# Performance work log

Measured on AMD Instinct MI355X. Metric: run time of the kernel, lower is better.

Reference implementation:

```python
import jax, jax.numpy as jnp
import numpy as np

B, N = 8, 512
EMBED, EDGE_D, FLAG_D = 256, 32, 32
NODE_NUM, EDGE_NUM, FLAG_NUM = 20000, 16, 4
IN_DIM = 2 * EMBED + 2 * FLAG_D + EDGE_D  # concat order: [head_emb, tail_emb, head_flag, tail_flag, edge]
NEG = -1e12


def setup_inputs() -> dict:
    key = jax.random.key(0)
    ks = jax.random.split(key, 16)
    s = 0.05
    return {
        "adjacent_matrix": jax.random.randint(ks[0], (B, N, N), 0, 2, dtype=jnp.int32),
        "head_nodes": jax.random.randint(ks[1], (B, N), 0, NODE_NUM, dtype=jnp.int32),
        "head_flag_bit_matrix": jax.random.randint(ks[2], (B, N), 0, FLAG_NUM, dtype=jnp.int32),
        "edge_type_matrix": jax.random.randint(ks[3], (B, N, N), 0, EDGE_NUM, dtype=jnp.int32),
        "node_emb": jax.random.normal(ks[4], (NODE_NUM, EMBED)) * s,
        "edge_emb": jax.random.normal(ks[5], (EDGE_NUM, EDGE_D)) * s,
        "flag_emb": jax.random.normal(ks[6], (FLAG_NUM, FLAG_D)) * s,
        "t1_w": jax.random.normal(ks[7], (EMBED, EMBED)) * s,
        "t1_b": jax.random.normal(ks[8], (EMBED,)) * s,
        "w1": jax.random.normal(ks[9], (IN_DIM,)) * s,
        "b1": jax.random.normal(ks[10], ()) * s,
        "t2_w": jax.random.normal(ks[11], (EMBED, EMBED)) * s,
        "t2_b": jax.random.normal(ks[12], (EMBED,)) * s,
        "w2": jax.random.normal(ks[13], (IN_DIM,)) * s,
        "b2": jax.random.normal(ks[14], ()) * s,
    }


def _leaky_relu(x):
    return jnp.where(x > 0, x, 0.1 * x)


def _gat_layer(h, f, e, adj, w, b):
    # Decompose Linear(concat([h_i, h_j, f_i, f_j, e_ij])) into per-part dot
    # products summed by broadcasting -> avoids the [B,N,N,IN_DIM] concat.
    D, F = h.shape[-1], f.shape[-1]
    wh, wt = w[:D], w[D:2 * D]
    wfh, wft = w[2 * D:2 * D + F], w[2 * D + F:2 * D + 2 * F]
    we = w[2 * D + 2 * F:]
    logit = ((h @ wh)[:, :, None] + (h @ wt)[:, None, :]
             + (f @ wfh)[:, :, None] + (f @ wft)[:, None, :]
             + jnp.einsum('bije,e->bij', e, we) + b)  # [B,N,N]
    logit = _leaky_relu(logit)
    logit = jnp.where(adj == 0, NEG, logit)
    att = jax.nn.softmax(logit, axis=1)  # softmax over head axis i
    # out[b,j] = sum_i att[b,i,j] * h[b,i]   (== bmm(att^T, h))
    return jnp.einsum('bij,bid->bjd', att, h)


def reference(adjacent_matrix, head_nodes, head_flag_bit_matrix, edge_type_matrix,
              node_emb, edge_emb, flag_emb,
              t1_w, t1_b, w1, b1, t2_w, t2_b, w2, b2):
    h = node_emb[head_nodes] @ t1_w.T + t1_b          # [B,N,D] (t1 projection)
    f = flag_emb[head_flag_bit_matrix]                # [B,N,F]
    e = edge_emb[edge_type_matrix]                    # [B,N,N,E]
    t = _gat_layer(h, f, e, adjacent_matrix, w1, b1)  # layer 1 aggregate
    t = jax.nn.sigmoid(t)
    h2 = t @ t2_w.T + t2_b                            # t2 projection
    return _gat_layer(h2, f, e, adjacent_matrix, w2, b2)
```

## Files before the change

kernel.cpp:

```cpp
#include <hip/hip_runtime.h>
#include <hip/hip_bf16.h>

#define BB 8
#define NN 512
#define DD 256
#define NROWS (BB*NN)
#define JT 16

using bf16x8 = __attribute__((ext_vector_type(8))) short;
using f32x4  = __attribute__((ext_vector_type(4))) float;
typedef unsigned short us_t;

__device__ __forceinline__ us_t f2bf(float x) {
    union { float f; unsigned int u; } v; v.f = x;
    unsigned int r = (v.u + 0x7fffu + ((v.u >> 16) & 1u)) >> 16;
    return (us_t)r;
}

__global__ __launch_bounds__(256) void prep_w(
    const float* __restrict__ w1f, const float* __restrict__ w2f,
    us_t* __restrict__ o1, us_t* __restrict__ o2)
{
    int i = blockIdx.x*1024 + threadIdx.x*4;
    float4 a = *(const float4*)(w1f + i);
    float4 b = *(const float4*)(w2f + i);
    ushort4 u;
    u.x = f2bf(a.x); u.y = f2bf(a.y); u.z = f2bf(a.z); u.w = f2bf(a.w);
    *(ushort4*)&o1[i] = u;
    u.x = f2bf(b.x); u.y = f2bf(b.y); u.z = f2bf(b.z); u.w = f2bf(b.w);
    *(ushort4*)&o2[i] = u;
}

__device__ __forceinline__ void lin_body(
    int bid, int t,
    const us_t* __restrict__ Wbf, const float* __restrict__ bias,
    const float* __restrict__ Xf, const int* __restrict__ idx,
    const float* __restrict__ wvec, const int* __restrict__ flagidx,
    const float* __restrict__ flag_emb,
    us_t* __restrict__ hT, float* __restrict__ aout, float* __restrict__ cout,
    float* redA, float* redC)
{
    const int wave = t >> 6, lane = t & 63;
    const int lrow = lane & 15, kg = lane >> 4;
    const int r0 = bid * 16;
    const int dw = wave * 64;

    const int arow = r0 + lrow;
    const int nid = idx ? idx[arow] : arow;

    f32x4 acc[4];
    #pragma unroll
    for (int n = 0; n < 4; ++n) acc[n] = (f32x4){0.f, 0.f, 0.f, 0.f};

    const float4* xr = (const float4*)(Xf + (size_t)nid * DD);
    #pragma unroll
    for (int ks = 0; ks < DD/32; ++ks) {
        float4 xa = xr[ks*8 + kg*2];
        float4 xb = xr[ks*8 + kg*2 + 1];
        bf16x8 af;
        af[0] = (short)f2bf(xa.x); af[1] = (short)f2bf(xa.y);
        af[2] = (short)f2bf(xa.z); af[3] = (short)f2bf(xa.w);
        af[4] = (short)f2bf(xb.x); af[5] = (short)f2bf(xb.y);
        af[6] = (short)f2bf(xb.z); af[7] = (short)f2bf(xb.w);
        #pragma unroll
        for (int n = 0; n < 4; ++n) {
            bf16x8 bfr = *(const bf16x8*)(Wbf + (size_t)(dw + n*16 + lrow)*DD
                                           + ks*32 + kg*8);
            acc[n] = __builtin_amdgcn_mfma_f32_16x16x32_bf16(af, bfr, acc[n], 0, 0, 0);
        }
    }

    const int b  = r0 >> 9;
    const int i0 = (r0 & 511) + kg*4;
    float pa[4] = {0.f,0.f,0.f,0.f}, pc[4] = {0.f,0.f,0.f,0.f};
    #pragma unroll
    for (int n = 0; n < 4; ++n) {
        int d = dw + n*16 + lrow;
        float bv = bias[d];
        float whd = wvec[d], wtd = wvec[256+d];
        ushort4 u;
        #pragma unroll
        for (int r = 0; r < 4; ++r) {
            float v = acc[n][r] + bv;
            ((us_t*)&u)[r] = f2bf(v);
            pa[r] += v * whd;
            pc[r] += v * wtd;
        }
        *(ushort4*)&hT[(size_t)b*DD*NN + (size_t)d*NN + i0] = u;
    }
    #pragma unroll
    for (int r = 0; r < 4; ++r) {
        #pragma unroll
        for (int m = 1; m < 16; m <<= 1) {
            pa[r] += __shfl_xor(pa[r], m);
            pc[r] += __shfl_xor(pc[r], m);
        }
    }
    if (lrow == 0) {
        #pragma unroll
        for (int r = 0; r < 4; ++r) {
            redA[wave*16 + kg*4 + r] = pa[r];
            redC[wave*16 + kg*4 + r] = pc[r];
        }
    }
    __syncthreads();
    if (t < 128) {
        const int m = t >> 3, sub = t & 7;
        const int fi = flagidx[r0 + m];
        float fa = 0.f, fc = 0.f;
        #pragma unroll
        for (int q = 0; q < 4; ++q) {
            int e = sub*4 + q;
            float fe = flag_emb[fi*32 + e];
            fa += fe * wvec[512 + e];
            fc += fe * wvec[544 + e];
        }
        #pragma unroll
        for (int mm = 1; mm < 8; mm <<= 1) {
            fa += __shfl_xor(fa, mm);
            fc += __shfl_xor(fc, mm);
        }
        if (sub == 0) {
            float sa = fa, sc = fc;
            #pragma unroll
            for (int wv = 0; wv < 4; ++wv) { sa += redA[wv*16 + m]; sc += redC[wv*16 + m]; }
            aout[r0 + m] = sa;
            cout[r0 + m] = sc;
        }
    }
}

__global__ __launch_bounds__(256) void k1(
    const us_t* __restrict__ Wb1, const float* __restrict__ bias1,
    const float* __restrict__ node_emb, const int* __restrict__ head_nodes,
    const float* __restrict__ wvec1, const int* __restrict__ flagidx,
    const float* __restrict__ flag_emb,
    us_t* __restrict__ hT, float* __restrict__ a1, float* __restrict__ c1,
    const int* __restrict__ adj, const int* __restrict__ et,
    unsigned char* __restrict__ pk)
{
    __shared__ float redA[64], redC[64];
    const int blk = blockIdx.x, t = threadIdx.x;
    if (blk < 256) {
        lin_body(blk, t, Wb1, bias1, node_emb, head_nodes,
                 wvec1, flagidx, flag_emb, hT, a1, c1, redA, redC);
    } else {
        int g = ((blk - 256)*256 + t)*4;
        int4 av = *(const int4*)(adj + g);
        int4 ev = *(const int4*)(et + g);
        uchar4 u;
        u.x = (unsigned char)((ev.x&15)|(av.x<<4));
        u.y = (unsigned char)((ev.y&15)|(av.y<<4));
        u.z = (unsigned char)((ev.z&15)|(av.z<<4));
        u.w = (unsigned char)((ev.w&15)|(av.w<<4));
        *(uchar4*)(pk + g) = u;
    }
}

__global__ __launch_bounds__(256) void attn1_lin2(
    const unsigned char* __restrict__ pk,
    const float* __restrict__ edge_emb, const float* __restrict__ w,
    const float* __restrict__ bptr,
    const float* __restrict__ a, const float* __restrict__ c,
    const us_t* __restrict__ hT,
    const us_t* __restrict__ Wb2, const float* __restrict__ bias2,
    const float* __restrict__ wvec2, const int* __restrict__ flagidx,
    const float* __restrict__ flag_emb,
    us_t* __restrict__ hT2, float* __restrict__ a2, float* __restrict__ c2)
{
    __shared__ __align__(16) float p[NN][JT+1];
    __shared__ __align__(16) us_t Pb[JT][NN+8];
    __shared__ __align__(16) us_t Sg[16][DD+8];
    __shared__ float as[NN];
    __shared__ float edot[16];
    __shared__ float cjs[JT];
    __shared__ float red[16][JT];
    __shared__ float mj[JT];
    __shared__ float invden[JT];
    __shared__ float redA[64], redC[64];

    const int t = threadIdx.x;
    const int b  = blockIdx.x >> 5;
    const int j0 = (blockIdx.x & 31) * JT;

    as[t]       = a[b*NN + t];
    as[256 + t] = a[b*NN + 256 + t];
    if (t < 16) {
        float s = 0.f;
        for (int e2 = 0; e2 < 32; ++e2)
            s += edge_emb[t*32 + e2] * w[576 + e2];
        edot[t] = s;
    } else if (t < 32) {
        cjs[t-16] = c[b*NN + j0 + (t-16)];
    }
    const float bias = bptr[0];
    __syncthreads();

    const unsigned char* pkb = pk + (size_t)b*NN*NN + j0;
    #pragma unroll
    for (int it = 0; it < NN*JT/1024; ++it) {
        int lid4 = (it*256 + t) * 4;
        int i = lid4 >> 4, jj = lid4 & 15;
        uchar4 u = *(const uchar4*)(pkb + (size_t)i*NN + jj);
        float base = as[i] + bias;
        unsigned char uv[4] = {u.x, u.y, u.z, u.w};
        #pragma unroll
        for (int q = 0; q < 4; ++q) {
            float l = base + cjs[jj+q] + edot[uv[q] & 15];
            l = (l > 0.f) ? l : 0.1f*l;
            p[i][jj+q] = (uv[q] >> 4) ? l : -1.0e30f;
        }
    }
    __syncthreads();

    const int j = t & 15, grp = t >> 4;
    float m = -3.0e38f;
    #pragma unroll
    for (int s = 0; s < 32; ++s) m = fmaxf(m, p[grp + s*16][j]);
    red[grp][j] = m;
    __syncthreads();
    if (t < 16) {
        float mm = red[0][t];
        for (int g2 = 1; g2 < 16; ++g2) mm = fmaxf(mm, red[g2][t]);
        mj[t] = mm;
    }
    __syncthreads();
    const float mmax = mj[j];
    float ssum = 0.f;
    #pragma unroll
    for (int s = 0; s < 32; ++s) {
        float v = __expf(p[grp + s*16][j] - mmax);
        p[grp + s*16][j] = v;
        ssum += v;
    }
    red[grp][j] = ssum;
    __syncthreads();
    if (t < 16) {
        float sm = 0.f;
        for (int g2 = 0; g2 < 16; ++g2) sm += red[g2][t];
        invden[t] = 1.f / sm;
    }
    __syncthreads();

    const float inv = invden[j];
    #pragma unroll
    for (int s = 0; s < 16; ++s) {
        int i = grp*2 + s*32;
        ushort2 u;
        u.x = f2bf(p[i  ][j] * inv);
        u.y = f2bf(p[i+1][j] * inv);
        *(ushort2*)&Pb[j][i] = u;
    }
    __syncthreads();

    const int wave = t >> 6, lane = t & 63;
    const int dw = wave * 64;
    const int lrow = lane & 15;
    const int kg   = lane >> 4;
    f32x4 acc[4];
    #pragma unroll
    for (int n = 0; n < 4; ++n) acc[n] = (f32x4){0.f,0.f,0.f,0.f};

    const us_t* hTb = hT + (size_t)b*DD*NN;
    const us_t* hp[4];
    #pragma unroll
    for (int n = 0; n < 4; ++n)
        hp[n] = hTb + (size_t)(dw + n*16 + lrow)*NN + kg*8;

    #pragma unroll 2
    for (int ks = 0; ks < NN/32; ++ks) {
        int k0 = ks*32;
        bf16x8 afr = *(const bf16x8*)&Pb[lrow][kg*8 + k0];
        #pragma unroll
        for (int n = 0; n < 4; ++n) {
            bf16x8 bfr = *(const bf16x8*)(hp[n] + k0);
            acc[n] = __builtin_amdgcn_mfma_f32_16x16x32_bf16(afr, bfr, acc[n], 0, 0, 0);
        }
    }

    #pragma unroll
    for (int n = 0; n < 4; ++n) {
        #pragma unroll
        for (int r = 0; r < 4; ++r) {
            float v = 1.f/(1.f + __expf(-acc[n][r]));
            Sg[kg*4 + r][dw + n*16 + lrow] = f2bf(v);
        }
    }
    __syncthreads();

    f32x4 acc2[4];
    #pragma unroll
    for (int n = 0; n < 4; ++n) acc2[n] = (f32x4){0.f,0.f,0.f,0.f};
    #pragma unroll
    for (int ks = 0; ks < DD/32; ++ks) {
        bf16x8 af2 = *(const bf16x8*)&Sg[lrow][ks*32 + kg*8];
        #pragma unroll
        for (int n = 0; n < 4; ++n) {
            bf16x8 bf2 = *(const bf16x8*)(Wb2 + (size_t)(dw + n*16 + lrow)*DD
                                           + ks*32 + kg*8);
            acc2[n] = __builtin_amdgcn_mfma_f32_16x16x32_bf16(af2, bf2, acc2[n], 0, 0, 0);
        }
    }

    const int r0 = b*NN + j0;
    const int i0 = j0 + kg*4;
    float pa[4] = {0.f,0.f,0.f,0.f}, pc[4] = {0.f,0.f,0.f,0.f};
    #pragma unroll
    for (int n = 0; n < 4; ++n) {
        int d = dw + n*16 + lrow;
        float bv = bias2[d];
        float whd = wvec2[d], wtd = wvec2[256+d];
        ushort4 u;
        #pragma unroll
        for (int r = 0; r < 4; ++r) {
            float v = acc2[n][r] + bv;
            ((us_t*)&u)[r] = f2bf(v);
            pa[r] += v * whd;
            pc[r] += v * wtd;
        }
        *(ushort4*)&hT2[(size_t)b*DD*NN + (size_t)d*NN + i0] = u;
    }
    #pragma unroll
    for (int r = 0; r < 4; ++r) {
        #pragma unroll
        for (int mk = 1; mk < 16; mk <<= 1) {
            pa[r] += __shfl_xor(pa[r], mk);
            pc[r] += __shfl_xor(pc[r], mk);
        }
    }
    if (lrow == 0) {
        #pragma unroll
        for (int r = 0; r < 4; ++r) {
            redA[wave*16 + kg*4 + r] = pa[r];
            redC[wave*16 + kg*4 + r] = pc[r];
        }
    }
    __syncthreads();
    if (t < 128) {
        const int mrow = t >> 3, sub = t & 7;
        const int fi = flagidx[r0 + mrow];
        float fa = 0.f, fc = 0.f;
        #pragma unroll
        for (int q = 0; q < 4; ++q) {
            int e = sub*4 + q;
            float fe = flag_emb[fi*32 + e];
            fa += fe * wvec2[512 + e];
            fc += fe * wvec2[544 + e];
        }
        #pragma unroll
        for (int mm = 1; mm < 8; mm <<= 1) {
            fa += __shfl_xor(fa, mm);
            fc += __shfl_xor(fc, mm);
        }
        if (sub == 0) {
            float sa = fa, sc = fc;
            #pragma unroll
            for (int wv = 0; wv < 4; ++wv) { sa += redA[wv*16 + mrow]; sc += redC[wv*16 + mrow]; }
            a2[r0 + mrow] = sa;
            c2[r0 + mrow] = sc;
        }
    }
}

__global__ __launch_bounds__(256) void attn2(
    const unsigned char* __restrict__ pk,
    const float* __restrict__ edge_emb, const float* __restrict__ w,
    const float* __restrict__ bptr,
    const float* __restrict__ a, const float* __restrict__ c,
    const us_t* __restrict__ hT,
    float* __restrict__ outf)
{
    __shared__ __align__(16) float p[NN][JT+1];
    __shared__ __align__(16) us_t Pb[JT][NN+8];
    __shared__ float as[NN];
    __shared__ float edot[16];
    __shared__ float cjs[JT];
    __shared__ float red[16][JT];
    __shared__ float mj[JT];
    __shared__ float invden[JT];

    const int t = threadIdx.x;
    const int b  = blockIdx.x >> 5;
    const int j0 = (blockIdx.x & 31) * JT;

    as[t]       = a[b*NN + t];
    as[256 + t] = a[b*NN + 256 + t];
    if (t < 16) {
        float s = 0.f;
        for (int e2 = 0; e2 < 32; ++e2)
            s += edge_emb[t*32 + e2] * w[576 + e2];
        edot[t] = s;
    } else if (t < 32) {
        cjs[t-16] = c[b*NN + j0 + (t-16)];
    }
    const float bias = bptr[0];
    __syncthreads();

    const unsigned char* pkb = pk + (size_t)b*NN*NN + j0;
    #pragma unroll
    for (int it = 0; it < NN*JT/1024; ++it) {
        int lid4 = (it*256 + t) * 4;
        int i = lid4 >> 4, jj = lid4 & 15;
        uchar4 u = *(const uchar4*)(pkb + (size_t)i*NN + jj);
        float base = as[i] + bias;
        unsigned char uv[4] = {u.x, u.y, u.z, u.w};
        #pragma unroll
        for (int q = 0; q < 4; ++q) {
            float l = base + cjs[jj+q] + edot[uv[q] & 15];
            l = (l > 0.f) ? l : 0.1f*l;
            p[i][jj+q] = (uv[q] >> 4) ? l : -1.0e30f;
        }
    }
    __syncthreads();

    const int j = t & 15, grp = t >> 4;
    float m = -3.0e38f;
    #pragma unroll
    for (int s = 0; s < 32; ++s) m = fmaxf(m, p[grp + s*16][j]);
    red[grp][j] = m;
    __syncthreads();
    if (t < 16) {
        float mm = red[0][t];
        for (int g2 = 1; g2 < 16; ++g2) mm = fmaxf(mm, red[g2][t]);
        mj[t] = mm;
    }
    __syncthreads();
    const float mmax = mj[j];
    float ssum = 0.f;
    #pragma unroll
    for (int s = 0; s < 32; ++s) {
        float v = __expf(p[grp + s*16][j] - mmax);
        p[grp + s*16][j] = v;
        ssum += v;
    }
    red[grp][j] = ssum;
    __syncthreads();
    if (t < 16) {
        float sm = 0.f;
        for (int g2 = 0; g2 < 16; ++g2) sm += red[g2][t];
        invden[t] = 1.f / sm;
    }
    __syncthreads();

    const float inv = invden[j];
    #pragma unroll
    for (int s = 0; s < 16; ++s) {
        int i = grp*2 + s*32;
        ushort2 u;
        u.x = f2bf(p[i  ][j] * inv);
        u.y = f2bf(p[i+1][j] * inv);
        *(ushort2*)&Pb[j][i] = u;
    }
    __syncthreads();

    const int wave = t >> 6, lane = t & 63;
    const int dw = wave * 64;
    const int lrow = lane & 15;
    const int kg   = lane >> 4;
    f32x4 acc[4];
    #pragma unroll
    for (int n = 0; n < 4; ++n) acc[n] = (f32x4){0.f,0.f,0.f,0.f};

    const us_t* hTb = hT + (size_t)b*DD*NN;
    const us_t* hp[4];
    #pragma unroll
    for (int n = 0; n < 4; ++n)
        hp[n] = hTb + (size_t)(dw + n*16 + lrow)*NN + kg*8;

    #pragma unroll 2
    for (int ks = 0; ks < NN/32; ++ks) {
        int k0 = ks*32;
        bf16x8 afr = *(const bf16x8*)&Pb[lrow][kg*8 + k0];
        #pragma unroll
        for (int n = 0; n < 4; ++n) {
            bf16x8 bfr = *(const bf16x8*)(hp[n] + k0);
            acc[n] = __builtin_amdgcn_mfma_f32_16x16x32_bf16(afr, bfr, acc[n], 0, 0, 0);
        }
    }

    #pragma unroll
    for (int n = 0; n < 4; ++n) {
        #pragma unroll
        for (int r = 0; r < 4; ++r) {
            int jj = j0 + kg*4 + r;
            int dd = dw + n*16 + lrow;
            outf[(size_t)(b*NN + jj)*DD + dd] = acc[n][r];
        }
    }
}

extern "C" void kernel_launch(void* const* d_in, const int* in_sizes, int n_in,
                              void* d_out, int out_size, void* d_ws, size_t ws_size,
                              hipStream_t stream) {
    (void)in_sizes; (void)n_in; (void)out_size; (void)ws_size;
    const int*   adj       = (const int*)d_in[0];
    const int*   head_nodes= (const int*)d_in[1];
    const int*   head_flag = (const int*)d_in[2];
    const int*   etype     = (const int*)d_in[3];
    const float* node_emb  = (const float*)d_in[4];
    const float* edge_emb  = (const float*)d_in[5];
    const float* flag_emb  = (const float*)d_in[6];
    const float* t1_w      = (const float*)d_in[7];
    const float* t1_b      = (const float*)d_in[8];
    const float* w1        = (const float*)d_in[9];
    const float* b1        = (const float*)d_in[10];
    const float* t2_w      = (const float*)d_in[11];
    const float* t2_b      = (const float*)d_in[12];
    const float* w2        = (const float*)d_in[13];
    const float* b2        = (const float*)d_in[14];

    us_t* hT1 = (us_t*)d_ws;
    us_t* hT2 = hT1 + (size_t)NROWS*DD;
    us_t* Wb1 = hT2 + (size_t)NROWS*DD;
    us_t* Wb2 = Wb1 + (size_t)DD*DD;
    unsigned char* pk = (unsigned char*)(Wb2 + (size_t)DD*DD);
    float* a1 = (float*)(pk + (size_t)BB*NN*NN);
    float* c1 = a1 + NROWS;
    float* a2 = c1 + NROWS;
    float* c2 = a2 + NROWS;

    prep_w<<<DD*DD/1024, 256, 0, stream>>>(t1_w, t2_w, Wb1, Wb2);
    k1<<<256 + BB*NN*NN/1024, 256, 0, stream>>>(
        Wb1, t1_b, node_emb, head_nodes, w1, head_flag, flag_emb,
        hT1, a1, c1, adj, etype, pk);
    attn1_lin2<<<BB*(NN/JT), 256, 0, stream>>>(
        pk, edge_emb, w1, b1, a1, c1, hT1,
        Wb2, t2_b, w2, head_flag, flag_emb, hT2, a2, c2);
    attn2<<<BB*(NN/JT), 256, 0, stream>>>(
        pk, edge_emb, w2, b2, a2, c2, hT2, (float*)d_out);
}
```

Measured before the change: 54.55 us.

## Fuse all stages into one cooperative persistent kernel with grid syncs

Merges the weight conversion, first projection, adjacency packing, both attention layers and the second projection into a single cooperative kernel of 256 blocks, separated by grid-wide barriers. t1_w is now converted to bf16 on the fly inside the first GEMM instead of in a separate prep kernel. The aim is to remove three kernel launch gaps and the associated tail effects. In exchange the work is bounded to 256 blocks, so the packing pass gets fewer threads, grid.sync adds its own cost, and shared-memory use limits how many blocks fit per CU.

```diff
diff --git a/kernel.cpp b/kernel.cpp
--- a/kernel.cpp
+++ b/kernel.cpp
@@ -1,5 +1,8 @@
 #include <hip/hip_runtime.h>
 #include <hip/hip_bf16.h>
+#include <hip/hip_cooperative_groups.h>
+
+namespace cg = cooperative_groups;
 
 #define BB 8
 #define NN 512
@@ -17,156 +20,17 @@
     return (us_t)r;
 }
 
-__global__ __launch_bounds__(256) void prep_w(
-    const float* __restrict__ w1f, const float* __restrict__ w2f,
-    us_t* __restrict__ o1, us_t* __restrict__ o2)
-{
-    int i = blockIdx.x*1024 + threadIdx.x*4;
-    float4 a = *(const float4*)(w1f + i);
-    float4 b = *(const float4*)(w2f + i);
-    ushort4 u;
-    u.x = f2bf(a.x); u.y = f2bf(a.y); u.z = f2bf(a.z); u.w = f2bf(a.w);
-    *(ushort4*)&o1[i] = u;
-    u.x = f2bf(b.x); u.y = f2bf(b.y); u.z = f2bf(b.z); u.w = f2bf(b.w);
-    *(ushort4*)&o2[i] = u;
-}
-
-__device__ __forceinline__ void lin_body(
-    int bid, int t,
-    const us_t* __restrict__ Wbf, const float* __restrict__ bias,
-    const float* __restrict__ Xf, const int* __restrict__ idx,
-    const float* __restrict__ wvec, const int* __restrict__ flagidx,
-    const float* __restrict__ flag_emb,
-    us_t* __restrict__ hT, float* __restrict__ aout, float* __restrict__ cout,
-    float* redA, float* redC)
-{
-    const int wave = t >> 6, lane = t & 63;
-    const int lrow = lane & 15, kg = lane >> 4;
-    const int r0 = bid * 16;
-    const int dw = wave * 64;
-
-    const int arow = r0 + lrow;
-    const int nid = idx ? idx[arow] : arow;
-
-    f32x4 acc[4];
-    #pragma unroll
-    for (int n = 0; n < 4; ++n) acc[n] = (f32x4){0.f, 0.f, 0.f, 0.f};
-
-    const float4* xr = (const float4*)(Xf + (size_t)nid * DD);
-    #pragma unroll
-    for (int ks = 0; ks < DD/32; ++ks) {
-        float4 xa = xr[ks*8 + kg*2];
-        float4 xb = xr[ks*8 + kg*2 + 1];
-        bf16x8 af;
-        af[0] = (short)f2bf(xa.x); af[1] = (short)f2bf(xa.y);
-        af[2] = (short)f2bf(xa.z); af[3] = (short)f2bf(xa.w);
-        af[4] = (short)f2bf(xb.x); af[5] = (short)f2bf(xb.y);
-        af[6] = (short)f2bf(xb.z); af[7] = (short)f2bf(xb.w);
-        #pragma unroll
-        for (int n = 0; n < 4; ++n) {
-            bf16x8 bfr = *(const bf16x8*)(Wbf + (size_t)(dw + n*16 + lrow)*DD
-                                           + ks*32 + kg*8);
-            acc[n] = __builtin_amdgcn_mfma_f32_16x16x32_bf16(af, bfr, acc[n], 0, 0, 0);
-        }
-    }
-
-    const int b  = r0 >> 9;
-    const int i0 = (r0 & 511) + kg*4;
-    float pa[4] = {0.f,0.f,0.f,0.f}, pc[4] = {0.f,0.f,0.f,0.f};
-    #pragma unroll
-    for (int n = 0; n < 4; ++n) {
-        int d = dw + n*16 + lrow;
-        float bv = bias[d];
-        float whd = wvec[d], wtd = wvec[256+d];
-        ushort4 u;
-        #pragma unroll
-        for (int r = 0; r < 4; ++r) {
-            float v = acc[n][r] + bv;
-            ((us_t*)&u)[r] = f2bf(v);
-            pa[r] += v * whd;
-            pc[r] += v * wtd;
-        }
-        *(ushort4*)&hT[(size_t)b*DD*NN + (size_t)d*NN + i0] = u;
-    }
-    #pragma unroll
-    for (int r = 0; r < 4; ++r) {
-        #pragma unroll
-        for (int m = 1; m < 16; m <<= 1) {
-            pa[r] += __shfl_xor(pa[r], m);
-            pc[r] += __shfl_xor(pc[r], m);
-        }
-    }
-    if (lrow == 0) {
-        #pragma unroll
-        for (int r = 0; r < 4; ++r) {
-            redA[wave*16 + kg*4 + r] = pa[r];
-            redC[wave*16 + kg*4 + r] = pc[r];
-        }
-    }
-    __syncthreads();
-    if (t < 128) {
-        const int m = t >> 3, sub = t & 7;
-        const int fi = flagidx[r0 + m];
-        float fa = 0.f, fc = 0.f;
-        #pragma unroll
-        for (int q = 0; q < 4; ++q) {
-            int e = sub*4 + q;
-            float fe = flag_emb[fi*32 + e];
-            fa += fe * wvec[512 + e];
-            fc += fe * wvec[544 + e];
-        }
-        #pragma unroll
-        for (int mm = 1; mm < 8; mm <<= 1) {
-            fa += __shfl_xor(fa, mm);
-            fc += __shfl_xor(fc, mm);
-        }
-        if (sub == 0) {
-            float sa = fa, sc = fc;
-            #pragma unroll
-            for (int wv = 0; wv < 4; ++wv) { sa += redA[wv*16 + m]; sc += redC[wv*16 + m]; }
-            aout[r0 + m] = sa;
-            cout[r0 + m] = sc;
-        }
-    }
-}
-
-__global__ __launch_bounds__(256) void k1(
-    const us_t* __restrict__ Wb1, const float* __restrict__ bias1,
-    const float* __restrict__ node_emb, const int* __restrict__ head_nodes,
-    const float* __restrict__ wvec1, const int* __restrict__ flagidx,
-    const float* __restrict__ flag_emb,
-    us_t* __restrict__ hT, float* __restrict__ a1, float* __restrict__ c1,
-    const int* __restrict__ adj, const int* __restrict__ et,
-    unsigned char* __restrict__ pk)
-{
-    __shared__ float redA[64], redC[64];
-    const int blk = blockIdx.x, t = threadIdx.x;
-    if (blk < 256) {
-        lin_body(blk, t, Wb1, bias1, node_emb, head_nodes,
-                 wvec1, flagidx, flag_emb, hT, a1, c1, redA, redC);
-    } else {
-        int g = ((blk - 256)*256 + t)*4;
-        int4 av = *(const int4*)(adj + g);
-        int4 ev = *(const int4*)(et + g);
-        uchar4 u;
-        u.x = (unsigned char)((ev.x&15)|(av.x<<4));
-        u.y = (unsigned char)((ev.y&15)|(av.y<<4));
-        u.z = (unsigned char)((ev.z&15)|(av.z<<4));
-        u.w = (unsigned char)((ev.w&15)|(av.w<<4));
-        *(uchar4*)(pk + g) = u;
-    }
-}
-
-__global__ __launch_bounds__(256) void attn1_lin2(
-    const unsigned char* __restrict__ pk,
-    const float* __restrict__ edge_emb, const float* __restrict__ w,
-    const float* __restrict__ bptr,
-    const float* __restrict__ a, const float* __restrict__ c,
-    const us_t* __restrict__ hT,
-    const us_t* __restrict__ Wb2, const float* __restrict__ bias2,
-    const float* __restrict__ wvec2, const int* __restrict__ flagidx,
-    const float* __restrict__ flag_emb,
-    us_t* __restrict__ hT2, float* __restrict__ a2, float* __restrict__ c2)
+struct MegaParams {
+    const int   *adj, *head_nodes, *head_flag, *etype;
+    const float *node_emb, *edge_emb, *flag_emb;
+    const float *t1_w, *t1_b, *w1, *b1, *t2_w, *t2_b, *w2, *b2;
+    us_t *hT1, *hT2, *Wb2;
+    unsigned char *pk;
+    float *a1, *c1, *a2, *c2;
+    float *outf;
+};
+
+__global__ __launch_bounds__(256) void mega(MegaParams P)
 {
     __shared__ __align__(16) float p[NN][JT+1];
     __shared__ __align__(16) us_t Pb[JT][NN+8];
@@ -179,312 +43,409 @@
     __shared__ float invden[JT];
     __shared__ float redA[64], redC[64];
 
-    const int t = threadIdx.x;
-    const int b  = blockIdx.x >> 5;
-    const int j0 = (blockIdx.x & 31) * JT;
-
-    as[t]       = a[b*NN + t];
-    as[256 + t] = a[b*NN + 256 + t];
-    if (t < 16) {
-        float s = 0.f;
-        for (int e2 = 0; e2 < 32; ++e2)
-            s += edge_emb[t*32 + e2] * w[576 + e2];
-        edot[t] = s;
-    } else if (t < 32) {
-        cjs[t-16] = c[b*NN + j0 + (t-16)];
+    const int t   = threadIdx.x;
+    const int bid = blockIdx.x;
+    const int wave = t >> 6, lane = t & 63;
+    const int lrow = lane & 15, kg = lane >> 4;
+    const int dw = wave * 64;
+
+    cg::grid_group grid = cg::this_grid();
+
+    #pragma unroll
+    for (int it = 0; it < 8; ++it) {
+        int e = ((bid*8 + it)*256 + t)*4;
+        int4 av = *(const int4*)(P.adj + e);
+        int4 ev = *(const int4*)(P.etype + e);
+        uchar4 u;
+        u.x = (unsigned char)((ev.x&15)|(av.x<<4));
+        u.y = (unsigned char)((ev.y&15)|(av.y<<4));
+        u.z = (unsigned char)((ev.z&15)|(av.z<<4));
+        u.w = (unsigned char)((ev.w&15)|(av.w<<4));
+        *(uchar4*)(P.pk + e) = u;
     }
-    const float bias = bptr[0];
-    __syncthreads();
-
-    const unsigned char* pkb = pk + (size_t)b*NN*NN + j0;
-    #pragma unroll
-    for (int it = 0; it < NN*JT/1024; ++it) {
-        int lid4 = (it*256 + t) * 4;
-        int i = lid4 >> 4, jj = lid4 & 15;
-        uchar4 u = *(const uchar4*)(pkb + (size_t)i*NN + jj);
-        float base = as[i] + bias;
-        unsigned char uv[4] = {u.x, u.y, u.z, u.w};
-        #pragma unroll
-        for (int q = 0; q < 4; ++q) {
-            float l = base + cjs[jj+q] + edot[uv[q] & 15];
-            l = (l > 0.f) ? l : 0.1f*l;
-            p[i][jj+q] = (uv[q] >> 4) ? l : -1.0e30f;
-        }
+    {
+        int wi = bid*256 + t;
+        P.Wb2[wi] = f2bf(P.t2_w[wi]);
     }
-    __syncthreads();
-
-    const int j = t & 15, grp = t >> 4;
-    float m = -3.0e38f;
-    #pragma unroll
-    for (int s = 0; s < 32; ++s) m = fmaxf(m, p[grp + s*16][j]);
-    red[grp][j] = m;
-    __syncthreads();
-    if (t < 16) {
-        float mm = red[0][t];
-        for (int g2 = 1; g2 < 16; ++g2) mm = fmaxf(mm, red[g2][t]);
-        mj[t] = mm;
+    {
+        const int r0 = bid * 16;
+        const int arow = r0 + lrow;
+        const int nid = P.head_nodes[arow];
+
+        f32x4 acc[4];
+        #pragma unroll
+        for (int n = 0; n < 4; ++n) acc[n] = (f32x4){0.f,0.f,0.f,0.f};
+
+        const float4* xr = (const float4*)(P.node_emb + (size_t)nid * DD);
+        #pragma unroll
+        for (int ks = 0; ks < DD/32; ++ks) {
+            float4 xa = xr[ks*8 + kg*2];
+            float4 xb = xr[ks*8 + kg*2 + 1];
+            bf16x8 af;
+            af[0] = (short)f2bf(xa.x); af[1] = (short)f2bf(xa.y);
+            af[2] = (short)f2bf(xa.z); af[3] = (short)f2bf(xa.w);
+            af[4] = (short)f2bf(xb.x); af[5] = (short)f2bf(xb.y);
+            af[6] = (short)f2bf(xb.z); af[7] = (short)f2bf(xb.w);
+            #pragma unroll
+            for (int n = 0; n < 4; ++n) {
+                const float4* wr = (const float4*)(P.t1_w + (size_t)(dw + n*16 + lrow)*DD
+                                                    + ks*32 + kg*8);
+                float4 wa = wr[0], wb = wr[1];
+                bf16x8 bfr;
+                bfr[0] = (short)f2bf(wa.x); bfr[1] = (short)f2bf(wa.y);
+                bfr[2] = (short)f2bf(wa.z); bfr[3] = (short)f2bf(wa.w);
+                bfr[4] = (short)f2bf(wb.x); bfr[5] = (short)f2bf(wb.y);
+                bfr[6] = (short)f2bf(wb.z); bfr[7] = (short)f2bf(wb.w);
+                acc[n] = __builtin_amdgcn_mfma_f32_16x16x32_bf16(af, bfr, acc[n], 0, 0, 0);
+            }
+        }
+
+        const int b  = r0 >> 9;
+        const int i0 = (r0 & 511) + kg*4;
+        float pa[4] = {0.f,0.f,0.f,0.f}, pc[4] = {0.f,0.f,0.f,0.f};
+        #pragma unroll
+        for (int n = 0; n < 4; ++n) {
+            int d = dw + n*16 + lrow;
+            float bv = P.t1_b[d];
+            float whd = P.w1[d], wtd = P.w1[256+d];
+            ushort4 u;
+            #pragma unroll
+            for (int r = 0; r < 4; ++r) {
+                float v = acc[n][r] + bv;
+                ((us_t*)&u)[r] = f2bf(v);
+                pa[r] += v * whd;
+                pc[r] += v * wtd;
+            }
+            *(ushort4*)&P.hT1[(size_t)b*DD*NN + (size_t)d*NN + i0] = u;
+        }
+        #pragma unroll
+        for (int r = 0; r < 4; ++r) {
+            #pragma unroll
+            for (int m = 1; m < 16; m <<= 1) {
+                pa[r] += __shfl_xor(pa[r], m);
+                pc[r] += __shfl_xor(pc[r], m);
+            }
+        }
+        if (lrow == 0) {
+            #pragma unroll
+            for (int r = 0; r < 4; ++r) {
+                redA[wave*16 + kg*4 + r] = pa[r];
+                redC[wave*16 + kg*4 + r] = pc[r];
+            }
+        }
+        __syncthreads();
+        if (t < 128) {
+            const int m = t >> 3, sub = t & 7;
+            const int fi = P.head_flag[r0 + m];
+            float fa = 0.f, fc = 0.f;
+            #pragma unroll
+            for (int q = 0; q < 4; ++q) {
+                int e = sub*4 + q;
+                float fe = P.flag_emb[fi*32 + e];
+                fa += fe * P.w1[512 + e];
+                fc += fe * P.w1[544 + e];
+            }
+            #pragma unroll
+            for (int mm = 1; mm < 8; mm <<= 1) {
+                fa += __shfl_xor(fa, mm);
+                fc += __shfl_xor(fc, mm);
+            }
+            if (sub == 0) {
+                float sa = fa, sc = fc;
+                #pragma unroll
+                for (int wv = 0; wv < 4; ++wv) { sa += redA[wv*16 + m]; sc += redC[wv*16 + m]; }
+                P.a1[r0 + m] = sa;
+                P.c1[r0 + m] = sc;
+            }
+        }
     }
-    __syncthreads();
-    const float mmax = mj[j];
-    float ssum = 0.f;
-    #pragma unroll
-    for (int s = 0; s < 32; ++s) {
-        float v = __expf(p[grp + s*16][j] - mmax);
-        p[grp + s*16][j] = v;
-        ssum += v;
+
+    grid.sync();
+
+    {
+        const int b  = bid >> 5;
+        const int j0 = (bid & 31) * JT;
+
+        as[t]       = P.a1[b*NN + t];
+        as[256 + t] = P.a1[b*NN + 256 + t];
+        if (t < 16) {
+            float s = 0.f;
+            for (int e2 = 0; e2 < 32; ++e2)
+                s += P.edge_emb[t*32 + e2] * P.w1[576 + e2];
+            edot[t] = s;
+        } else if (t < 32) {
+            cjs[t-16] = P.c1[b*NN + j0 + (t-16)];
+        }
+        const float bias = P.b1[0];
+        __syncthreads();
+
+        const unsigned char* pkb = P.pk + (size_t)b*NN*NN + j0;
+        #pragma unroll
+        for (int it = 0; it < NN*JT/1024; ++it) {
+            int lid4 = (it*256 + t) * 4;
+            int i = lid4 >> 4, jj = lid4 & 15;
+            uchar4 u = *(const uchar4*)(pkb + (size_t)i*NN + jj);
+            float base = as[i] + bias;
+            unsigned char uv[4] = {u.x, u.y, u.z, u.w};
+            #pragma unroll
+            for (int q = 0; q < 4; ++q) {
+                float l = base + cjs[jj+q] + edot[uv[q] & 15];
+                l = (l > 0.f) ? l : 0.1f*l;
+                p[i][jj+q] = (uv[q] >> 4) ? l : -1.0e30f;
+            }
+        }
+        __syncthreads();
+
+        const int j = t & 15, grp = t >> 4;
+        float m = -3.0e38f;
+        #pragma unroll
+        for (int s = 0; s < 32; ++s) m = fmaxf(m, p[grp + s*16][j]);
+        red[grp][j] = m;
+        __syncthreads();
+        if (t < 16) {
+            float mm = red[0][t];
+            for (int g2 = 1; g2 < 16; ++g2) mm = fmaxf(mm, red[g2][t]);
+            mj[t] = mm;
+        }
+        __syncthreads();
+        const float mmax = mj[j];
+        float ssum = 0.f;
+        #pragma unroll
+        for (int s = 0; s < 32; ++s) {
+            float v = __expf(p[grp + s*16][j] - mmax);
+            p[grp + s*16][j] = v;
+            ssum += v;
+        }
+        red[grp][j] = ssum;
+        __syncthreads();
+        if (t < 16) {
+            float sm = 0.f;
+            for (int g2 = 0; g2 < 16; ++g2) sm += red[g2][t];
+            invden[t] = 1.f / sm;
+        }
+        __syncthreads();
+
+        const float inv = invden[j];
+        #pragma unroll
+        for (int s = 0; s < 16; ++s) {
+            int i = grp*2 + s*32;
+            ushort2 u;
+            u.x = f2bf(p[i  ][j] * inv);
+            u.y = f2bf(p[i+1][j] * inv);
+            *(ushort2*)&Pb[j][i] = u;
+        }
+        __syncthreads();
+
+        f32x4 acc[4];
+        #pragma unroll
+        for (int n = 0; n < 4; ++n) acc[n] = (f32x4){0.f,0.f,0.f,0.f};
+
+        const us_t* hTb = P.hT1 + (size_t)b*DD*NN;
+        const us_t* hp[4];
+        #pragma unroll
+        for (int n = 0; n < 4; ++n)
+            hp[n] = hTb + (size_t)(dw + n*16 + lrow)*NN + kg*8;
+
+        #pragma unroll 2
+        for (int ks = 0; ks < NN/32; ++ks) {
+            int k0 = ks*32;
+            bf16x8 afr = *(const bf16x8*)&Pb[lrow][kg*8 + k0];
+            #pragma unroll
+            for (int n = 0; n < 4; ++n) {
+                bf16x8 bfr = *(const bf16x8*)(hp[n] + k0);
+                acc[n] = __builtin_amdgcn_mfma_f32_16x16x32_bf16(afr, bfr, acc[n], 0, 0, 0);
+            }
+        }
+
+        #pragma unroll
+        for (int n = 0; n < 4; ++n) {
+            #pragma unroll
+            for (int r = 0; r < 4; ++r) {
+                float v = 1.f/(1.f + __expf(-acc[n][r]));
+                Sg[kg*4 + r][dw + n*16 + lrow] = f2bf(v);
+            }
+        }
+        __syncthreads();
+
+        f32x4 acc2[4];
+        #pragma unroll
+        for (int n = 0; n < 4; ++n) acc2[n] = (f32x4){0.f,0.f,0.f,0.f};
+        #pragma unroll
+        for (int ks = 0; ks < DD/32; ++ks) {
+            bf16x8 af2 = *(const bf16x8*)&Sg[lrow][ks*32 + kg*8];
+            #pragma unroll
+            for (int n = 0; n < 4; ++n) {
+                bf16x8 bf2 = *(const bf16x8*)(P.Wb2 + (size_t)(dw + n*16 + lrow)*DD
+                                               + ks*32 + kg*8);
+                acc2[n] = __builtin_amdgcn_mfma_f32_16x16x32_bf16(af2, bf2, acc2[n], 0, 0, 0);
+            }
+        }
+
+        const int r0 = b*NN + j0;
+        const int i0 = j0 + kg*4;
+        float pa[4] = {0.f,0.f,0.f,0.f}, pc[4] = {0.f,0.f,0.f,0.f};
+        #pragma unroll
+        for (int n = 0; n < 4; ++n) {
+            int d = dw + n*16 + lrow;
+            float bv = P.t2_b[d];
+            float whd = P.w2[d], wtd = P.w2[256+d];
+            ushort4 u;
+            #pragma unroll
+            for (int r = 0; r < 4; ++r) {
+                float v = acc2[n][r] + bv;
+                ((us_t*)&u)[r] = f2bf(v);
+                pa[r] += v * whd;
+                pc[r] += v * wtd;
+            }
+            *(ushort4*)&P.hT2[(size_t)b*DD*NN + (size_t)d*NN + i0] = u;
+        }
+        #pragma unroll
+        for (int r = 0; r < 4; ++r) {
+            #pragma unroll
+            for (int mk = 1; mk < 16; mk <<= 1) {
+                pa[r] += __shfl_xor(pa[r], mk);
+                pc[r] += __shfl_xor(pc[r], mk);
+            }
+        }
+        if (lrow == 0) {
+            #pragma unroll
+            for (int r = 0; r < 4; ++r) {
+                redA[wave*16 + kg*4 + r] = pa[r];
+                redC[wave*16 + kg*4 + r] = pc[r];
+            }
+        }
+        __syncthreads();
+        if (t < 128) {
+            const int mrow = t >> 3, sub = t & 7;
+            const int fi = P.head_flag[r0 + mrow];
+            float fa = 0.f, fc = 0.f;
+            #pragma unroll
+            for (int q = 0; q < 4; ++q) {
+                int e = sub*4 + q;
+                float fe = P.flag_emb[fi*32 + e];
+                fa += fe * P.w2[512 + e];
+                fc += fe * P.w2[544 + e];
+            }
+            #pragma unroll
+            for (int mm = 1; mm < 8; mm <<= 1) {
+                fa += __shfl_xor(fa, mm);
+                fc += __shfl_xor(fc, mm);
+            }
+            if (sub == 0) {
+                float sa = fa, sc = fc;
+                #pragma unroll
+                for (int wv = 0; wv < 4; ++wv) { sa += redA[wv*16 + mrow]; sc += redC[wv*16 + mrow]; }
+                P.a2[r0 + mrow] = sa;
+                P.c2[r0 + mrow] = sc;
+            }
+        }
     }
-    red[grp][j] = ssum;
-    __syncthreads();
-    if (t < 16) {
-        float sm = 0.f;
-        for (int g2 = 0; g2 < 16; ++g2) sm += red[g2][t];
-        invden[t] = 1.f / sm;
-    }
-    __syncthreads();
-
-    const float inv = invden[j];
-    #pragma unroll
-    for (int s = 0; s < 16; ++s) {
-        int i = grp*2 + s*32;
-        ushort2 u;
-        u.x = f2bf(p[i  ][j] * inv);
-        u.y = f2bf(p[i+1][j] * inv);
-        *(ushort2*)&Pb[j][i] = u;
-    }
-    __syncthreads();
-
-    const int wave = t >> 6, lane = t & 63;
-    const int dw = wave * 64;
-    const int lrow = lane & 15;
-    const int kg   = lane >> 4;
-    f32x4 acc[4];
-    #pragma unroll
-    for (int n = 0; n < 4; ++n) acc[n] = (f32x4){0.f,0.f,0.f,0.f};
-
-    const us_t* hTb = hT + (size_t)b*DD*NN;
-    const us_t* hp[4];
-    #pragma unroll
-    for (int n = 0; n < 4; ++n)
-        hp[n] = hTb + (size_t)(dw + n*16 + lrow)*NN + kg*8;
-
-    #pragma unroll 2
-    for (int ks = 0; ks < NN/32; ++ks) {
-        int k0 = ks*32;
-        bf16x8 afr = *(const bf16x8*)&Pb[lrow][kg*8 + k0];
+
+    grid.sync();
+
+    {
+        const int b  = bid >> 5;
+        const int j0 = (bid & 31) * JT;
+
+        as[t]       = P.a2[b*NN + t];
+        as[256 + t] = P.a2[b*NN + 256 + t];
+        if (t < 16) {
+            float s = 0.f;
+            for (int e2 = 0; e2 < 32; ++e2)
+                s += P.edge_emb[t*32 + e2] * P.w2[576 + e2];
+            edot[t] = s;
+        } else if (t < 32) {
+            cjs[t-16] = P.c2[b*NN + j0 + (t-16)];
+        }
+        const float bias = P.b2[0];
+        __syncthreads();
+
+        const unsigned char* pkb = P.pk + (size_t)b*NN*NN + j0;
+        #pragma unroll
+        for (int it = 0; it < NN*JT/1024; ++it) {
+            int lid4 = (it*256 + t) * 4;
+            int i = lid4 >> 4, jj = lid4 & 15;
+            uchar4 u = *(const uchar4*)(pkb + (size_t)i*NN + jj);
+            float base = as[i] + bias;
+            unsigned char uv[4] = {u.x, u.y, u.z, u.w};
+            #pragma unroll
+            for (int q = 0; q < 4; ++q) {
+                float l = base + cjs[jj+q] + edot[uv[q] & 15];
+                l = (l > 0.f) ? l : 0.1f*l;
+                p[i][jj+q] = (uv[q] >> 4) ? l : -1.0e30f;
+            }
+        }
+        __syncthreads();
+
+        const int j = t & 15, grp = t >> 4;
+        float m = -3.0e38f;
+        #pragma unroll
+        for (int s = 0; s < 32; ++s) m = fmaxf(m, p[grp + s*16][j]);
+        red[grp][j] = m;
+        __syncthreads();
+        if (t < 16) {
+            float mm = red[0][t];
+            for (int g2 = 1; g2 < 16; ++g2) mm = fmaxf(mm, red[g2][t]);
+            mj[t] = mm;
+        }
+        __syncthreads();
+        const float mmax = mj[j];
+        float ssum = 0.f;
+        #pragma unroll
+        for (int s = 0; s < 32; ++s) {
+            float v = __expf(p[grp + s*16][j] - mmax);
+            p[grp + s*16][j] = v;
+            ssum += v;
+        }
+        red[grp][j] = ssum;
+        __syncthreads();
+        if (t < 16) {
+            float sm = 0.f;
+            for (int g2 = 0; g2 < 16; ++g2) sm += red[g2][t];
+            invden[t] = 1.f / sm;
+        }
+        __syncthreads();
+
+        const float inv = invden[j];
+        #pragma unroll
+        for (int s = 0; s < 16; ++s) {
+            int i = grp*2 + s*32;
+            ushort2 u;
+            u.x = f2bf(p[i  ][j] * inv);
+            u.y = f2bf(p[i+1][j] * inv);
+            *(ushort2*)&Pb[j][i] = u;
+        }
+        __syncthreads();
+
+        f32x4 acc[4];
+        #pragma unroll
+        for (int n = 0; n < 4; ++n) acc[n] = (f32x4){0.f,0.f,0.f,0.f};
+
+        const us_t* hTb = P.hT2 + (size_t)b*DD*NN;
+        const us_t* hp[4];
+        #pragma unroll
+        for (int n = 0; n < 4; ++n)
+            hp[n] = hTb + (size_t)(dw + n*16 + lrow)*NN + kg*8;
+
+        #pragma unroll 2
+        for (int ks = 0; ks < NN/32; ++ks) {
+            int k0 = ks*32;
+            bf16x8 afr = *(const bf16x8*)&Pb[lrow][kg*8 + k0];
+            #pragma unroll
+            for (int n = 0; n < 4; ++n) {
+                bf16x8 bfr = *(const bf16x8*)(hp[n] + k0);
+                acc[n] = __builtin_amdgcn_mfma_f32_16x16x32_bf16(afr, bfr, acc[n], 0, 0, 0);
+            }
+        }
+
         #pragma unroll
         for (int n = 0; n < 4; ++n) {
-            bf16x8 bfr = *(const bf16x8*)(hp[n] + k0);
-            acc[n] = __builtin_amdgcn_mfma_f32_16x16x32_bf16(afr, bfr, acc[n], 0, 0, 0);
-        }
-    }
-
-    #pragma unroll
-    for (int n = 0; n < 4; ++n) {
-        #pragma unroll
-        for (int r = 0; r < 4; ++r) {
-            float v = 1.f/(1.f + __expf(-acc[n][r]));
-            Sg[kg*4 + r][dw + n*16 + lrow] = f2bf(v);
-        }
-    }
-    __syncthreads();
-
-    f32x4 acc2[4];
-    #pragma unroll
-    for (int n = 0; n < 4; ++n) acc2[n] = (f32x4){0.f,0.f,0.f,0.f};
-    #pragma unroll
-    for (int ks = 0; ks < DD/32; ++ks) {
-        bf16x8 af2 = *(const bf16x8*)&Sg[lrow][ks*32 + kg*8];
-        #pragma unroll
-        for (int n = 0; n < 4; ++n) {
-            bf16x8 bf2 = *(const bf16x8*)(Wb2 + (size_t)(dw + n*16 + lrow)*DD
-                                           + ks*32 + kg*8);
-            acc2[n] = __builtin_amdgcn_mfma_f32_16x16x32_bf16(af2, bf2, acc2[n], 0, 0, 0);
-        }
-    }
-
-    const int r0 = b*NN + j0;
-    const int i0 = j0 + kg*4;
-    float pa[4] = {0.f,0.f,0.f,0.f}, pc[4] = {0.f,0.f,0.f,0.f};
-    #pragma unroll
-    for (int n = 0; n < 4; ++n) {
-        int d = dw + n*16 + lrow;
-        float bv = bias2[d];
-        float whd = wvec2[d], wtd = wvec2[256+d];
-        ushort4 u;
-        #pragma unroll
-        for (int r = 0; r < 4; ++r) {
-            float v = acc2[n][r] + bv;
-            ((us_t*)&u)[r] = f2bf(v);
-            pa[r] += v * whd;
-            pc[r] += v * wtd;
-        }
-        *(ushort4*)&hT2[(size_t)b*DD*NN + (size_t)d*NN + i0] = u;
-    }
-    #pragma unroll
-    for (int r = 0; r < 4; ++r) {
-        #pragma unroll
-        for (int mk = 1; mk < 16; mk <<= 1) {
-            pa[r] += __shfl_xor(pa[r], mk);
-            pc[r] += __shfl_xor(pc[r], mk);
-        }
-    }
-    if (lrow == 0) {
-        #pragma unroll
-        for (int r = 0; r < 4; ++r) {
-            redA[wave*16 + kg*4 + r] = pa[r];
-            redC[wave*16 + kg*4 + r] = pc[r];
-        }
-    }
-    __syncthreads();
-    if (t < 128) {
-        const int mrow = t >> 3, sub = t & 7;
-        const int fi = flagidx[r0 + mrow];
-        float fa = 0.f, fc = 0.f;
-        #pragma unroll
-        for (int q = 0; q < 4; ++q) {
-            int e = sub*4 + q;
-            float fe = flag_emb[fi*32 + e];
-            fa += fe * wvec2[512 + e];
-            fc += fe * wvec2[544 + e];
-        }
-        #pragma unroll
-        for (int mm = 1; mm < 8; mm <<= 1) {
-            fa += __shfl_xor(fa, mm);
-            fc += __shfl_xor(fc, mm);
-        }
-        if (sub == 0) {
-            float sa = fa, sc = fc;
-            #pragma unroll
-            for (int wv = 0; wv < 4; ++wv) { sa += redA[wv*16 + mrow]; sc += redC[wv*16 + mrow]; }
-            a2[r0 + mrow] = sa;
-            c2[r0 + mrow] = sc;
-        }
-    }
-}
-
-__global__ __launch_bounds__(256) void attn2(
-    const unsigned char* __restrict__ pk,
-    const float* __restrict__ edge_emb, const float* __restrict__ w,
-    const float* __restrict__ bptr,
-    const float* __restrict__ a, const float* __restrict__ c,
-    const us_t* __restrict__ hT,
-    float* __restrict__ outf)
-{
-    __shared__ __align__(16) float p[NN][JT+1];
-    __shared__ __align__(16) us_t Pb[JT][NN+8];
-    __shared__ float as[NN];
-    __shared__ float edot[16];
-    __shared__ float cjs[JT];
-    __shared__ float red[16][JT];
-    __shared__ float mj[JT];
-    __shared__ float invden[JT];
-
-    const int t = threadIdx.x;
-    const int b  = blockIdx.x >> 5;
-    const int j0 = (blockIdx.x & 31) * JT;
-
-    as[t]       = a[b*NN + t];
-    as[256 + t] = a[b*NN + 256 + t];
-    if (t < 16) {
-        float s = 0.f;
-        for (int e2 = 0; e2 < 32; ++e2)
-            s += edge_emb[t*32 + e2] * w[576 + e2];
-        edot[t] = s;
-    } else if (t < 32) {
-        cjs[t-16] = c[b*NN + j0 + (t-16)];
-    }
-    const float bias = bptr[0];
-    __syncthreads();
-
-    const unsigned char* pkb = pk + (size_t)b*NN*NN + j0;
-    #pragma unroll
-    for (int it = 0; it < NN*JT/1024; ++it) {
-        int lid4 = (it*256 + t) * 4;
-        int i = lid4 >> 4, jj = lid4 & 15;
-        uchar4 u = *(const uchar4*)(pkb + (size_t)i*NN + jj);
-        float base = as[i] + bias;
-        unsigned char uv[4] = {u.x, u.y, u.z, u.w};
-        #pragma unroll
-        for (int q = 0; q < 4; ++q) {
-            float l = base + cjs[jj+q] + edot[uv[q] & 15];
-            l = (l > 0.f) ? l : 0.1f*l;
-            p[i][jj+q] = (uv[q] >> 4) ? l : -1.0e30f;
-        }
-    }
-    __syncthreads();
-
-    const int j = t & 15, grp = t >> 4;
-    float m = -3.0e38f;
-    #pragma unroll
-    for (int s = 0; s < 32; ++s) m = fmaxf(m, p[grp + s*16][j]);
-    red[grp][j] = m;
-    __syncthreads();
-    if (t < 16) {
-        float mm = red[0][t];
-        for (int g2 = 1; g2 < 16; ++g2) mm = fmaxf(mm, red[g2][t]);
-        mj[t] = mm;
-    }
-    __syncthreads();
-    const float mmax = mj[j];
-    float ssum = 0.f;
-    #pragma unroll
-    for (int s = 0; s < 32; ++s) {
-        float v = __expf(p[grp + s*16][j] - mmax);
-        p[grp + s*16][j] = v;
-        ssum += v;
-    }
-    red[grp][j] = ssum;
-    __syncthreads();
-    if (t < 16) {
-        float sm = 0.f;
-        for (int g2 = 0; g2 < 16; ++g2) sm += red[g2][t];
-        invden[t] = 1.f / sm;
-    }
-    __syncthreads();
-
-    const float inv = invden[j];
-    #pragma unroll
-    for (int s = 0; s < 16; ++s) {
-        int i = grp*2 + s*32;
-        ushort2 u;
-        u.x = f2bf(p[i  ][j] * inv);
-        u.y = f2bf(p[i+1][j] * inv);
-        *(ushort2*)&Pb[j][i] = u;
-    }
-    __syncthreads();
-
-    const int wave = t >> 6, lane = t & 63;
-    const int dw = wave * 64;
-    const int lrow = lane & 15;
-    const int kg   = lane >> 4;
-    f32x4 acc[4];
-    #pragma unroll
-    for (int n = 0; n < 4; ++n) acc[n] = (f32x4){0.f,0.f,0.f,0.f};
-
-    const us_t* hTb = hT + (size_t)b*DD*NN;
-    const us_t* hp[4];
-    #pragma unroll
-    for (int n = 0; n < 4; ++n)
-        hp[n] = hTb + (size_t)(dw + n*16 + lrow)*NN + kg*8;
-
-    #pragma unroll 2
-    for (int ks = 0; ks < NN/32; ++ks) {
-        int k0 = ks*32;
-        bf16x8 afr = *(const bf16x8*)&Pb[lrow][kg*8 + k0];
-        #pragma unroll
-        for (int n = 0; n < 4; ++n) {
-            bf16x8 bfr = *(const bf16x8*)(hp[n] + k0);
-            acc[n] = __builtin_amdgcn_mfma_f32_16x16x32_bf16(afr, bfr, acc[n], 0, 0, 0);
-        }
-    }
-
-    #pragma unroll
-    for (int n = 0; n < 4; ++n) {
-        #pragma unroll
-        for (int r = 0; r < 4; ++r) {
-            int jj = j0 + kg*4 + r;
-            int dd = dw + n*16 + lrow;
-            outf[(size_t)(b*NN + jj)*DD + dd] = acc[n][r];
+            #pragma unroll
+            for (int r = 0; r < 4; ++r) {
+                int jj = j0 + kg*4 + r;
+                int dd = dw + n*16 + lrow;
+                P.outf[(size_t)(b*NN + jj)*DD + dd] = acc[n][r];
+            }
         }
     }
 }
@@ -493,39 +454,37 @@
                               void* d_out, int out_size, void* d_ws, size_t ws_size,
                               hipStream_t stream) {
     (void)in_sizes; (void)n_in; (void)out_size; (void)ws_size;
-    const int*   adj       = (const int*)d_in[0];
-    const int*   head_nodes= (const int*)d_in[1];
-    const int*   head_flag = (const int*)d_in[2];
-    const int*   etype     = (const int*)d_in[3];
-    const float* node_emb  = (const float*)d_in[4];
-    const float* edge_emb  = (const float*)d_in[5];
-    const float* flag_emb  = (const float*)d_in[6];
-    const float* t1_w      = (const float*)d_in[7];
-    const float* t1_b      = (const float*)d_in[8];
-    const float* w1        = (const float*)d_in[9];
-    const float* b1        = (const float*)d_in[10];
-    const float* t2_w      = (const float*)d_in[11];
-    const float* t2_b      = (const float*)d_in[12];
-    const float* w2        = (const float*)d_in[13];
-    const float* b2        = (const float*)d_in[14];
 
     us_t* hT1 = (us_t*)d_ws;
     us_t* hT2 = hT1 + (size_t)NROWS*DD;
-    us_t* Wb1 = hT2 + (size_t)NROWS*DD;
-    us_t* Wb2 = Wb1 + (size_t)DD*DD;
+    us_t* Wb2 = hT2 + (size_t)NROWS*DD;
     unsigned char* pk = (unsigned char*)(Wb2 + (size_t)DD*DD);
     float* a1 = (float*)(pk + (size_t)BB*NN*NN);
     float* c1 = a1 + NROWS;
     float* a2 = c1 + NROWS;
     float* c2 = a2 + NROWS;
 
-    prep_w<<<DD*DD/1024, 256, 0, stream>>>(t1_w, t2_w, Wb1, Wb2);
-    k1<<<256 + BB*NN*NN/1024, 256, 0, stream>>>(
-        Wb1, t1_b, node_emb, head_nodes, w1, head_flag, flag_emb,
-        hT1, a1, c1, adj, etype, pk);
-    attn1_lin2<<<BB*(NN/JT), 256, 0, stream>>>(
-        pk, edge_emb, w1, b1, a1, c1, hT1,
-        Wb2, t2_b, w2, head_flag, flag_emb, hT2, a2, c2);
-    attn2<<<BB*(NN/JT), 256, 0, stream>>>(
-        pk, edge_emb, w2, b2, a2, c2, hT2, (float*)d_out);
+    MegaParams P;
+    P.adj        = (const int*)d_in[0];
+    P.head_nodes = (const int*)d_in[1];
+    P.head_flag  = (const int*)d_in[2];
+    P.etype      = (const int*)d_in[3];
+    P.node_emb   = (const float*)d_in[4];
+    P.edge_emb   = (const float*)d_in[5];
+    P.flag_emb   = (const float*)d_in[6];
+    P.t1_w       = (const float*)d_in[7];
+    P.t1_b       = (const float*)d_in[8];
+    P.w1         = (const float*)d_in[9];
+    P.b1         = (const float*)d_in[10];
+    P.t2_w       = (const float*)d_in[11];
+    P.t2_b       = (const float*)d_in[12];
+    P.w2         = (const float*)d_in[13];
+    P.b2         = (const float*)d_in[14];
+    P.hT1 = hT1; P.hT2 = hT2; P.Wb2 = Wb2; P.pk = pk;
+    P.a1 = a1; P.c1 = c1; P.a2 = a2; P.c2 = c2;
+    P.outf = (float*)d_out;
+
+    void* args[] = { &P };
+    hipLaunchCooperativeKernel((const void*)mega, dim3(256), dim3(256),
+                               args, 0, stream);
 }
```

Result: slower. 118.6 us (+117.5%).
